# Kernel optimization log

Measured on AMD Instinct MI355X. Metric: run time of the kernel, lower is better.

Reference implementation:

```python
import jax, jax.numpy as jnp
import numpy as np
import math

B, L, D, H = 2, 2048, 1024, 16
DK = D // H

def setup_inputs() -> dict:
    key = jax.random.key(0)
    ks = jax.random.split(key, 12)
    s = 1.0 / math.sqrt(D)
    inp = {
        "Q": jax.random.normal(ks[0], (B, L, D), jnp.float32),
        "K": jax.random.normal(ks[1], (B, L, D), jnp.float32),
        "V": jax.random.normal(ks[2], (B, L, D), jnp.float32),
        "mask": jnp.tril(jnp.ones((L, L), jnp.bool_))[None, None],  # [1,1,L,L] causal
        "Wq_w": jax.random.normal(ks[3], (D, D), jnp.float32) * s,
        "Wq_b": jnp.zeros((D,), jnp.float32),
        "Wk_w": jax.random.normal(ks[4], (D, D), jnp.float32) * s,
        "Wk_b": jnp.zeros((D,), jnp.float32),
        "Wv_w": jax.random.normal(ks[5], (D, D), jnp.float32) * s,
        "Wv_b": jnp.zeros((D,), jnp.float32),
        "fc_w": jax.random.normal(ks[6], (D, D), jnp.float32) * s,
        "fc_b": jnp.zeros((D,), jnp.float32),
    }
    return inp

def reference(Q, K, V, mask, Wq_w, Wq_b, Wk_w, Wk_b, Wv_w, Wv_b, fc_w, fc_b):
    # torch Linear: y = x @ W.T + b
    def split_heads(x):
        return x.reshape(B, L, H, DK).transpose(0, 2, 1, 3)  # [B,H,L,DK]
    q = split_heads(Q @ Wq_w.T + Wq_b)
    k = split_heads(K @ Wk_w.T + Wk_b)
    v = split_heads(V @ Wv_w.T + Wv_b)
    scores = jnp.einsum("bhqd,bhkd->bhqk", q, k) / math.sqrt(DK)
    scores = jnp.where(mask, scores, jnp.float32(-1e9))
    attn = jax.nn.softmax(scores, axis=-1)
    out = jnp.einsum("bhqk,bhkd->bhqd", attn, v)
    out = out.transpose(0, 2, 1, 3).reshape(B, L, D)
    return out @ fc_w.T + fc_b
```

## Files before the change

### kernel.cpp

```cpp
#include <hip/hip_runtime.h>
#include <hip/hip_bf16.h>
#include <math.h>

typedef __attribute__((ext_vector_type(8))) short short8;
typedef __attribute__((ext_vector_type(4))) short short4v;
typedef __attribute__((ext_vector_type(4))) float float4v;
typedef __attribute__((ext_vector_type(2))) unsigned int uint2v;

static constexpr int Bc = 2, Lc = 2048, Dc = 1024, Hc = 16;
static constexpr float C1 = 0.125f * 1.44269504088896f;
static constexpr float C2 = -8.0f * 1.44269504088896f;

__device__ __forceinline__ short f2bf(float x) {
    unsigned int b = __float_as_uint(x);
    return (short)((b + 0x7FFFu + ((b >> 16) & 1u)) >> 16);
}

__device__ __forceinline__ void gld16(const void* g, void* l) {
    __builtin_amdgcn_global_load_lds(
        (const __attribute__((address_space(1))) unsigned int*)g,
        (__attribute__((address_space(3))) unsigned int*)l, 16, 0, 0);
}

__global__ __launch_bounds__(256) void cvt_all(
    const float* q, const float* k, const float* v,
    const float* wq, const float* wk, const float* wv, const float* fw,
    short* qo, short* ko, short* vo,
    short* wqo, short* wko, short* wvo, short* fwo)
{
    const int z = blockIdx.y;
    const float* s; short* d; int n;
    switch (z) {
        case 0: s = q;  d = qo;  n = Bc*Lc*Dc; break;
        case 1: s = k;  d = ko;  n = Bc*Lc*Dc; break;
        case 2: s = v;  d = vo;  n = Bc*Lc*Dc; break;
        case 3: s = wq; d = wqo; n = Dc*Dc; break;
        case 4: s = wk; d = wko; n = Dc*Dc; break;
        case 5: s = wv; d = wvo; n = Dc*Dc; break;
        default: s = fw; d = fwo; n = Dc*Dc; break;
    }
    const int idx = (blockIdx.x * 256 + threadIdx.x) * 8;
    if (idx >= n) return;
    float4 lo = *reinterpret_cast<const float4*>(s + idx);
    float4 hi = *reinterpret_cast<const float4*>(s + idx + 4);
    short8 o = short8{f2bf(lo.x), f2bf(lo.y), f2bf(lo.z), f2bf(lo.w),
                      f2bf(hi.x), f2bf(hi.y), f2bf(hi.z), f2bf(hi.w)};
    *reinterpret_cast<short8*>(d + idx) = o;
}

struct GemmCtx {
    int lane, w, wm, wn, quad, l16, bm0, bn0, lrow, loct;
};
__device__ __forceinline__ void gemm_core(
    const short* __restrict__ A, const short* __restrict__ Bt,
    short* As, short* Bs, const GemmCtx& c, float4v acc[4][4])
{
    const int K = Dc;
    for (int k0 = 0; k0 < K; k0 += 32) {
#pragma unroll
        for (int rep = 0; rep < 2; ++rep) {
            const int rb = (c.w + 4 * rep) * 16;
            gld16(A  + (size_t)(c.bm0 + rb + c.lrow) * K + k0 + c.loct * 8, &As[rb * 32]);
            gld16(Bt + (size_t)(c.bn0 + rb + c.lrow) * K + k0 + c.loct * 8, &Bs[rb * 32]);
        }
        __syncthreads();
        short8 af[4], bf[4];
#pragma unroll
        for (int i = 0; i < 4; ++i)
            af[i] = *reinterpret_cast<const short8*>(&As[(c.wm * 64 + i * 16 + c.l16) * 32 + c.quad * 8]);
#pragma unroll
        for (int j = 0; j < 4; ++j)
            bf[j] = *reinterpret_cast<const short8*>(&Bs[(c.wn * 64 + j * 16 + c.l16) * 32 + c.quad * 8]);
#pragma unroll
        for (int i = 0; i < 4; ++i)
#pragma unroll
            for (int j = 0; j < 4; ++j)
                acc[i][j] = __builtin_amdgcn_mfma_f32_16x16x32_bf16(af[i], bf[j], acc[i][j], 0, 0, 0);
        __syncthreads();
    }
}
__device__ __forceinline__ GemmCtx make_ctx() {
    GemmCtx c;
    const int tid = threadIdx.x;
    c.lane = tid & 63; c.w = tid >> 6;
    c.wm = c.w >> 1;   c.wn = c.w & 1;
    c.quad = c.lane >> 4; c.l16 = c.lane & 15;
    c.bm0 = blockIdx.y * 128; c.bn0 = blockIdx.x * 128;
    c.lrow = c.lane >> 2; c.loct = c.lane & 3;
    return c;
}

__global__ __launch_bounds__(256, 2) void qkv_gemm(
    const short* __restrict__ Qb, const short* __restrict__ Kb, const short* __restrict__ Vb,
    const short* __restrict__ Wq, const short* __restrict__ Wk, const short* __restrict__ Wv,
    const float* __restrict__ bq, const float* __restrict__ bk, const float* __restrict__ bv,
    short* __restrict__ q_ws, short* __restrict__ k_ws, short* __restrict__ vT_ws)
{
    __shared__ short As[128 * 32];
    __shared__ short Bs[128 * 32];
    const int z = blockIdx.z;
    const short* A    = (z == 0) ? Qb : (z == 1) ? Kb : Vb;
    const short* Bt   = (z == 0) ? Wq : (z == 1) ? Wk : Wv;
    const float* bias = (z == 0) ? bq : (z == 1) ? bk : bv;

    GemmCtx c = make_ctx();
    float4v acc[4][4] = {};
    gemm_core(A, Bt, As, Bs, c, acc);

    if (z < 2) {
        short* C = (z == 0) ? q_ws : k_ws;
#pragma unroll
        for (int j = 0; j < 4; ++j) {
            const int col = c.bn0 + c.wn * 64 + j * 16 + c.l16;
            const float bv2 = bias[col];
#pragma unroll
            for (int i = 0; i < 4; ++i)
#pragma unroll
                for (int r = 0; r < 4; ++r) {
                    const int row = c.bm0 + c.wm * 64 + i * 16 + c.quad * 4 + r;
                    C[(size_t)row * Dc + col] = f2bf(acc[i][j][r] + bv2);
                }
        }
    } else {
#pragma unroll
        for (int j = 0; j < 4; ++j) {
            const int col = c.bn0 + c.wn * 64 + j * 16 + c.l16;
            const float bv2 = bias[col];
            const int hh = col >> 6, d = col & 63;
#pragma unroll
            for (int i = 0; i < 4; ++i) {
                const int row0 = c.bm0 + c.wm * 64 + i * 16 + c.quad * 4;
                const int bb = row0 >> 11, l = row0 & 2047;
                short4v o4;
#pragma unroll
                for (int r = 0; r < 4; ++r) o4[r] = f2bf(acc[i][j][r] + bv2);
                *reinterpret_cast<short4v*>(
                    &vT_ws[((size_t)((bb * 16 + hh) * 64 + d)) * Lc + l]) = o4;
            }
        }
    }
}

__global__ __launch_bounds__(256, 2) void out_gemm(
    const short* __restrict__ A, const short* __restrict__ Bt,
    const float* __restrict__ bias, float* __restrict__ C)
{
    __shared__ short As[128 * 32];
    __shared__ short Bs[128 * 32];
    GemmCtx c = make_ctx();
    float4v acc[4][4] = {};
    gemm_core(A, Bt, As, Bs, c, acc);
#pragma unroll
    for (int j = 0; j < 4; ++j) {
        const int col = c.bn0 + c.wn * 64 + j * 16 + c.l16;
        const float bv2 = bias[col];
#pragma unroll
        for (int i = 0; i < 4; ++i)
#pragma unroll
            for (int r = 0; r < 4; ++r) {
                const int row = c.bm0 + c.wm * 64 + i * 16 + c.quad * 4 + r;
                C[(size_t)row * Dc + col] = acc[i][j][r] + bv2;
            }
    }
}

__global__ __launch_bounds__(256, 4) void attn_flash5(
    const short* __restrict__ q_ws,
    const short* __restrict__ k_ws,
    const short* __restrict__ vT_ws,
    short* __restrict__ o_ws)
{
    __shared__ short Ks[2][64 * 64];
    __shared__ short Vs[2][64 * 64];

    const int tid  = threadIdx.x;
    const int lane = tid & 63;
    const int w    = tid >> 6;
    const int quad = lane >> 4;
    const int l16  = lane & 15;
    const int l7   = l16 & 7;

    const int id = blockIdx.x;
    const int g  = id >> 8;
    const int s  = (id >> 5) & 7;
    const int bh = id & 31;
    const int qi = (g == 0) ? (31 - s) : (g == 1) ? (23 - s)
                 : (g == 2) ? s        : (8 + s);
    const int b  = bh >> 4, h = bh & 15;

    const int srow = lane >> 3;
    const int soct = lane & 7;
    const size_t khead  = (size_t)(b * Lc) * Dc + h * 64;
    const size_t vthead = (size_t)(bh * 64) * Lc;
    const int xoct0 = quad ^ l7;
    const int xoct1 = (4 + quad) ^ l7;

    const short onev = (l16 == 0) ? (short)0x3F80 : (short)0;
    const short4v vb4 = short4v{onev, onev, onev, onev};

    auto stage = [&](int tile, int buf) {
#pragma unroll
        for (int rep = 0; rep < 2; ++rep) {
            const int issue = w * 2 + rep;
            const int grow = issue * 8 + srow;
            const int goct = soct ^ (grow & 7);
            gld16(k_ws + khead + (size_t)(tile * 64 + grow) * Dc + goct * 8,
                  &Ks[buf][issue * 512]);
            gld16(vT_ws + vthead + (size_t)grow * Lc + tile * 64 + goct * 8,
                  &Vs[buf][issue * 512]);
        }
    };

    const int q0   = qi * 64;
    const int qw0  = q0 + w * 16;
    const int qrow = qw0 + l16;

    short8 qf[2];
    {
        const size_t base = ((size_t)(b * Lc + qw0 + l16)) * Dc + h * 64;
        qf[0] = *reinterpret_cast<const short8*>(&q_ws[base + quad * 8]);
        qf[1] = *reinterpret_cast<const short8*>(&q_ws[base + 32 + quad * 8]);
    }

    float4v o_acc[5] = {};

    stage(0, 0);

#pragma unroll 1
    for (int kb = 0; kb <= qi; ++kb) {
        const int cur = kb & 1;
        if (kb < qi) {
            stage(kb + 1, cur ^ 1);
            asm volatile("s_waitcnt vmcnt(4)" ::: "memory");
        } else {
            asm volatile("s_waitcnt vmcnt(0)" ::: "memory");
        }
        __builtin_amdgcn_s_barrier();
        asm volatile("" ::: "memory");

        const short* Kc = &Ks[cur][0];
        const short* Vc = &Vs[cur][0];

#pragma unroll
        for (int t = 0; t < 4; ++t) {
            if (kb * 64 + t * 16 <= qw0 + 15) {
                short8 kf0 = *reinterpret_cast<const short8*>(&Kc[(t * 16 + l16) * 64 + xoct0 * 8]);
                short8 kf1 = *reinterpret_cast<const short8*>(&Kc[(t * 16 + l16) * 64 + xoct1 * 8]);
                float4v sv = {};
                sv = __builtin_amdgcn_mfma_f32_16x16x32_bf16(kf0, qf[0], sv, 0, 0, 0);
                sv = __builtin_amdgcn_mfma_f32_16x16x32_bf16(kf1, qf[1], sv, 0, 0, 0);

                short4v vb[4];
#pragma unroll
                for (int dt = 0; dt < 4; ++dt)
                    vb[dt] = *reinterpret_cast<const short4v*>(
                        &Vc[(dt * 16 + l16) * 64 + ((2 * t + (quad >> 1)) ^ l7) * 8 + (quad & 1) * 4]);

                const int kbase = kb * 64 + t * 16 + quad * 4;
                unsigned u[4];
                if (kb * 64 + t * 16 + 15 <= qw0) {
#pragma unroll
                    for (int r = 0; r < 4; ++r)
                        u[r] = __float_as_uint(exp2f(fmaf(sv[r], C1, C2)));
                } else {
#pragma unroll
                    for (int r = 0; r < 4; ++r) {
                        const float pv = (kbase + r <= qrow)
                                       ? exp2f(fmaf(sv[r], C1, C2)) : 0.f;
                        u[r] = __float_as_uint(pv);
                    }
                }
                const uint2v pu = {(u[1] & 0xFFFF0000u) | (u[0] >> 16),
                                   (u[3] & 0xFFFF0000u) | (u[2] >> 16)};
                const short4v pa = __builtin_bit_cast(short4v, pu);

#pragma unroll
                for (int dt = 0; dt < 4; ++dt)
                    o_acc[dt] = __builtin_amdgcn_mfma_f32_16x16x16bf16_1k(pa, vb[dt], o_acc[dt], 0, 0, 0);
                o_acc[4] = __builtin_amdgcn_mfma_f32_16x16x16bf16_1k(pa, vb4, o_acc[4], 0, 0, 0);
            }
        }
        asm volatile("" ::: "memory");
        __builtin_amdgcn_s_barrier();
    }

#pragma unroll
    for (int r = 0; r < 4; ++r) {
        const float lsum = __shfl(o_acc[4][r], quad << 4, 64);
        const float inv = 1.f / lsum;
        const int qr = qw0 + quad * 4 + r;
#pragma unroll
        for (int dt = 0; dt < 4; ++dt)
            o_ws[((size_t)(b * Lc + qr)) * Dc + h * 64 + dt * 16 + l16] =
                f2bf(o_acc[dt][r] * inv);
    }
}

extern "C" void kernel_launch(void* const* d_in, const int* in_sizes, int n_in,
                              void* d_out, int out_size, void* d_ws, size_t ws_size,
                              hipStream_t stream)
{
    const float* Q = (const float*)d_in[0];
    const float* K = (const float*)d_in[1];
    const float* V = (const float*)d_in[2];

    int w0 = -1;
    for (int i = 3; i + 8 <= n_in; ++i) {
        bool ok = true;
        for (int j = 0; j < 4 && ok; ++j)
            ok = (in_sizes[i + 2 * j] == Dc * Dc) && (in_sizes[i + 2 * j + 1] == Dc);
        if (ok) { w0 = i; break; }
    }
    if (w0 < 0) w0 = (n_in >= 12) ? 4 : 3;

    const float* Wq_w = (const float*)d_in[w0 + 0];
    const float* Wq_b = (const float*)d_in[w0 + 1];
    const float* Wk_w = (const float*)d_in[w0 + 2];
    const float* Wk_b = (const float*)d_in[w0 + 3];
    const float* Wv_w = (const float*)d_in[w0 + 4];
    const float* Wv_b = (const float*)d_in[w0 + 5];
    const float* fc_w = (const float*)d_in[w0 + 6];
    const float* fc_b = (const float*)d_in[w0 + 7];
    float* out = (float*)d_out;

    const size_t nel = (size_t)Bc * Lc * Dc;
    const size_t nw  = (size_t)Dc * Dc;
    short* p = (short*)d_ws;
    short* xq   = p;  p += nel;
    short* xk   = p;  p += nel;
    short* xv   = p;  p += nel;
    short* wqb  = p;  p += nw;
    short* wkb  = p;  p += nw;
    short* wvb  = p;  p += nw;
    short* fwb  = p;  p += nw;
    short* q_ws = p;  p += nel;
    short* k_ws = p;  p += nel;
    short* vT_ws= p;  p += nel;
    short* a_ws = xq;

    cvt_all<<<dim3(2048, 7), 256, 0, stream>>>(
        Q, K, V, Wq_w, Wk_w, Wv_w, fc_w, xq, xk, xv, wqb, wkb, wvb, fwb);

    qkv_gemm<<<dim3(8, 32, 3), 256, 0, stream>>>(
        xq, xk, xv, wqb, wkb, wvb, Wq_b, Wk_b, Wv_b, q_ws, k_ws, vT_ws);

    attn_flash5<<<dim3(1024), 256, 0, stream>>>(q_ws, k_ws, vT_ws, a_ws);

    out_gemm<<<dim3(8, 32), 256, 0, stream>>>(a_ws, fwb, fc_b, out);
}
```

Measured before the change: 234.7 us.

## Split attention key tiles across two wave groups and shrink GEMM N-tile

The attention kernel now runs 512 threads in two 4-wave groups. Each group processes alternating 64-key tiles into its own LDS buffer, and the partial outputs and row sums are combined through LDS at the end. This replaces the single-group double-buffered prefetch loop, adding parallelism per query tile but dropping the load/compute overlap. Separately, the QKV and output GEMMs move from 128x128 to 128x64 tiles with a higher occupancy hint, doubling the block count to fill the GPU better at the cost of more A-tile reloads. The tighter launch bounds (512 threads, 8 blocks) may squeeze registers.

```diff
diff --git a/kernel.cpp b/kernel.cpp
--- a/kernel.cpp
+++ b/kernel.cpp
@@ -51,30 +51,31 @@
 struct GemmCtx {
     int lane, w, wm, wn, quad, l16, bm0, bn0, lrow, loct;
 };
-__device__ __forceinline__ void gemm_core(
+__device__ __forceinline__ void gemm_core64(
     const short* __restrict__ A, const short* __restrict__ Bt,
-    short* As, short* Bs, const GemmCtx& c, float4v acc[4][4])
+    short* As, short* Bs, const GemmCtx& c, float4v acc[4][2])
 {
     const int K = Dc;
     for (int k0 = 0; k0 < K; k0 += 32) {
 #pragma unroll
         for (int rep = 0; rep < 2; ++rep) {
             const int rb = (c.w + 4 * rep) * 16;
-            gld16(A  + (size_t)(c.bm0 + rb + c.lrow) * K + k0 + c.loct * 8, &As[rb * 32]);
-            gld16(Bt + (size_t)(c.bn0 + rb + c.lrow) * K + k0 + c.loct * 8, &Bs[rb * 32]);
-        }
+            gld16(A + (size_t)(c.bm0 + rb + c.lrow) * K + k0 + c.loct * 8, &As[rb * 32]);
+        }
+        gld16(Bt + (size_t)(c.bn0 + c.w * 16 + c.lrow) * K + k0 + c.loct * 8,
+              &Bs[c.w * 16 * 32]);
         __syncthreads();
-        short8 af[4], bf[4];
+        short8 af[4], bf[2];
 #pragma unroll
         for (int i = 0; i < 4; ++i)
             af[i] = *reinterpret_cast<const short8*>(&As[(c.wm * 64 + i * 16 + c.l16) * 32 + c.quad * 8]);
 #pragma unroll
-        for (int j = 0; j < 4; ++j)
-            bf[j] = *reinterpret_cast<const short8*>(&Bs[(c.wn * 64 + j * 16 + c.l16) * 32 + c.quad * 8]);
+        for (int j = 0; j < 2; ++j)
+            bf[j] = *reinterpret_cast<const short8*>(&Bs[(c.wn * 32 + j * 16 + c.l16) * 32 + c.quad * 8]);
 #pragma unroll
         for (int i = 0; i < 4; ++i)
 #pragma unroll
-            for (int j = 0; j < 4; ++j)
+            for (int j = 0; j < 2; ++j)
                 acc[i][j] = __builtin_amdgcn_mfma_f32_16x16x32_bf16(af[i], bf[j], acc[i][j], 0, 0, 0);
         __syncthreads();
     }
@@ -85,33 +86,33 @@
     c.lane = tid & 63; c.w = tid >> 6;
     c.wm = c.w >> 1;   c.wn = c.w & 1;
     c.quad = c.lane >> 4; c.l16 = c.lane & 15;
-    c.bm0 = blockIdx.y * 128; c.bn0 = blockIdx.x * 128;
+    c.bm0 = blockIdx.y * 128; c.bn0 = blockIdx.x * 64;
     c.lrow = c.lane >> 2; c.loct = c.lane & 3;
     return c;
 }
 
-__global__ __launch_bounds__(256, 2) void qkv_gemm(
+__global__ __launch_bounds__(256, 4) void qkv_gemm(
     const short* __restrict__ Qb, const short* __restrict__ Kb, const short* __restrict__ Vb,
     const short* __restrict__ Wq, const short* __restrict__ Wk, const short* __restrict__ Wv,
     const float* __restrict__ bq, const float* __restrict__ bk, const float* __restrict__ bv,
     short* __restrict__ q_ws, short* __restrict__ k_ws, short* __restrict__ vT_ws)
 {
     __shared__ short As[128 * 32];
-    __shared__ short Bs[128 * 32];
+    __shared__ short Bs[64 * 32];
     const int z = blockIdx.z;
     const short* A    = (z == 0) ? Qb : (z == 1) ? Kb : Vb;
     const short* Bt   = (z == 0) ? Wq : (z == 1) ? Wk : Wv;
     const float* bias = (z == 0) ? bq : (z == 1) ? bk : bv;
 
     GemmCtx c = make_ctx();
-    float4v acc[4][4] = {};
-    gemm_core(A, Bt, As, Bs, c, acc);
+    float4v acc[4][2] = {};
+    gemm_core64(A, Bt, As, Bs, c, acc);
 
     if (z < 2) {
         short* C = (z == 0) ? q_ws : k_ws;
 #pragma unroll
-        for (int j = 0; j < 4; ++j) {
-            const int col = c.bn0 + c.wn * 64 + j * 16 + c.l16;
+        for (int j = 0; j < 2; ++j) {
+            const int col = c.bn0 + c.wn * 32 + j * 16 + c.l16;
             const float bv2 = bias[col];
 #pragma unroll
             for (int i = 0; i < 4; ++i)
@@ -123,8 +124,8 @@
         }
     } else {
 #pragma unroll
-        for (int j = 0; j < 4; ++j) {
-            const int col = c.bn0 + c.wn * 64 + j * 16 + c.l16;
+        for (int j = 0; j < 2; ++j) {
+            const int col = c.bn0 + c.wn * 32 + j * 16 + c.l16;
             const float bv2 = bias[col];
             const int hh = col >> 6, d = col & 63;
 #pragma unroll
@@ -141,18 +142,18 @@
     }
 }
 
-__global__ __launch_bounds__(256, 2) void out_gemm(
+__global__ __launch_bounds__(256, 4) void out_gemm(
     const short* __restrict__ A, const short* __restrict__ Bt,
     const float* __restrict__ bias, float* __restrict__ C)
 {
     __shared__ short As[128 * 32];
-    __shared__ short Bs[128 * 32];
+    __shared__ short Bs[64 * 32];
     GemmCtx c = make_ctx();
-    float4v acc[4][4] = {};
-    gemm_core(A, Bt, As, Bs, c, acc);
-#pragma unroll
-    for (int j = 0; j < 4; ++j) {
-        const int col = c.bn0 + c.wn * 64 + j * 16 + c.l16;
+    float4v acc[4][2] = {};
+    gemm_core64(A, Bt, As, Bs, c, acc);
+#pragma unroll
+    for (int j = 0; j < 2; ++j) {
+        const int col = c.bn0 + c.wn * 32 + j * 16 + c.l16;
         const float bv2 = bias[col];
 #pragma unroll
         for (int i = 0; i < 4; ++i)
@@ -164,18 +165,19 @@
     }
 }
 
-__global__ __launch_bounds__(256, 4) void attn_flash5(
+__global__ __launch_bounds__(512, 8) void attn_flash6(
     const short* __restrict__ q_ws,
     const short* __restrict__ k_ws,
     const short* __restrict__ vT_ws,
     short* __restrict__ o_ws)
 {
-    __shared__ short Ks[2][64 * 64];
-    __shared__ short Vs[2][64 * 64];
+    __shared__ __align__(16) short KVs[2][2][64 * 64];
 
     const int tid  = threadIdx.x;
     const int lane = tid & 63;
     const int w    = tid >> 6;
+    const int grp  = w >> 2;
+    const int wq   = w & 3;
     const int quad = lane >> 4;
     const int l16  = lane & 15;
     const int l7   = l16 & 7;
@@ -198,21 +200,21 @@
     const short onev = (l16 == 0) ? (short)0x3F80 : (short)0;
     const short4v vb4 = short4v{onev, onev, onev, onev};
 
-    auto stage = [&](int tile, int buf) {
+    auto stage = [&](int tile) {
 #pragma unroll
         for (int rep = 0; rep < 2; ++rep) {
-            const int issue = w * 2 + rep;
+            const int issue = wq * 2 + rep;
             const int grow = issue * 8 + srow;
             const int goct = soct ^ (grow & 7);
             gld16(k_ws + khead + (size_t)(tile * 64 + grow) * Dc + goct * 8,
-                  &Ks[buf][issue * 512]);
+                  &KVs[grp][0][issue * 512]);
             gld16(vT_ws + vthead + (size_t)grow * Lc + tile * 64 + goct * 8,
-                  &Vs[buf][issue * 512]);
+                  &KVs[grp][1][issue * 512]);
         }
     };
 
     const int q0   = qi * 64;
-    const int qw0  = q0 + w * 16;
+    const int qw0  = q0 + wq * 16;
     const int qrow = qw0 + l16;
 
     short8 qf[2];
@@ -224,22 +226,18 @@
 
     float4v o_acc[5] = {};
 
-    stage(0, 0);
+    const int nsi = (qi >> 1) + 1;
 
 #pragma unroll 1
-    for (int kb = 0; kb <= qi; ++kb) {
-        const int cur = kb & 1;
-        if (kb < qi) {
-            stage(kb + 1, cur ^ 1);
-            asm volatile("s_waitcnt vmcnt(4)" ::: "memory");
-        } else {
-            asm volatile("s_waitcnt vmcnt(0)" ::: "memory");
-        }
+    for (int si = 0; si < nsi; ++si) {
+        const int kb = 2 * si + grp;
+        stage(kb);
+        asm volatile("s_waitcnt vmcnt(0)" ::: "memory");
         __builtin_amdgcn_s_barrier();
         asm volatile("" ::: "memory");
 
-        const short* Kc = &Ks[cur][0];
-        const short* Vc = &Vs[cur][0];
+        const short* Kc = &KVs[grp][0][0];
+        const short* Vc = &KVs[grp][1][0];
 
 #pragma unroll
         for (int t = 0; t < 4; ++t) {
@@ -284,15 +282,27 @@
         __builtin_amdgcn_s_barrier();
     }
 
-#pragma unroll
-    for (int r = 0; r < 4; ++r) {
-        const float lsum = __shfl(o_acc[4][r], quad << 4, 64);
-        const float inv = 1.f / lsum;
-        const int qr = qw0 + quad * 4 + r;
-#pragma unroll
-        for (int dt = 0; dt < 4; ++dt)
-            o_ws[((size_t)(b * Lc + qr)) * Dc + h * 64 + dt * 16 + l16] =
-                f2bf(o_acc[dt][r] * inv);
+    float4v* cmbv = reinterpret_cast<float4v*>(&KVs[0][0][0]);
+    if (grp == 1) {
+#pragma unroll
+        for (int dt = 0; dt < 5; ++dt)
+            cmbv[dt * 256 + wq * 64 + lane] = o_acc[dt];
+    }
+    __syncthreads();
+    if (grp == 0) {
+#pragma unroll
+        for (int dt = 0; dt < 5; ++dt)
+            o_acc[dt] += cmbv[dt * 256 + wq * 64 + lane];
+#pragma unroll
+        for (int r = 0; r < 4; ++r) {
+            const float lsum = __shfl(o_acc[4][r], quad << 4, 64);
+            const float inv = 1.f / lsum;
+            const int qr = qw0 + quad * 4 + r;
+#pragma unroll
+            for (int dt = 0; dt < 4; ++dt)
+                o_ws[((size_t)(b * Lc + qr)) * Dc + h * 64 + dt * 16 + l16] =
+                    f2bf(o_acc[dt][r] * inv);
+        }
     }
 }
 
@@ -341,10 +351,10 @@
     cvt_all<<<dim3(2048, 7), 256, 0, stream>>>(
         Q, K, V, Wq_w, Wk_w, Wv_w, fc_w, xq, xk, xv, wqb, wkb, wvb, fwb);
 
-    qkv_gemm<<<dim3(8, 32, 3), 256, 0, stream>>>(
+    qkv_gemm<<<dim3(16, 32, 3), 256, 0, stream>>>(
         xq, xk, xv, wqb, wkb, wvb, Wq_b, Wk_b, Wv_b, q_ws, k_ws, vT_ws);
 
-    attn_flash5<<<dim3(1024), 256, 0, stream>>>(q_ws, k_ws, vT_ws, a_ws);
-
-    out_gemm<<<dim3(8, 32), 256, 0, stream>>>(a_ws, fwb, fc_b, out);
-}
+    attn_flash6<<<dim3(1024), 512, 0, stream>>>(q_ws, k_ws, vT_ws, a_ws);
+
+    out_gemm<<<dim3(16, 32), 256, 0, stream>>>(a_ws, fwb, fc_b, out);
+}
```

After: 255.0 us. +8.6%, slower.

## Split long causal attention rows across two blocks and combine partial sums

Applied to the files above, without the earlier changes.

Query tiles in the upper half (qi>=16) now have their key range split between two blocks. Each block writes unnormalized partial accumulators and row sums to a float workspace, and a new combine kernel adds the two halves and normalizes. This works because the softmax uses a fixed max offset, so partials add directly. The change also separates full off-diagonal tiles from the diagonal tile so the mask check only runs on the diagonal, raises launch bounds to 5 blocks, and adds s_setprio around MFMA groups. The cost is an extra kernel launch plus the global round-trip for the partials, in exchange for less tail imbalance across the grid.

```diff
diff --git a/kernel.cpp b/kernel.cpp
--- a/kernel.cpp
+++ b/kernel.cpp
@@ -164,11 +164,12 @@
     }
 }
 
-__global__ __launch_bounds__(256, 4) void attn_flash5(
+__global__ __launch_bounds__(256, 5) void attn_flash8(
     const short* __restrict__ q_ws,
     const short* __restrict__ k_ws,
     const short* __restrict__ vT_ws,
-    short* __restrict__ o_ws)
+    short* __restrict__ o_ws,
+    float4v* __restrict__ pbuf)
 {
     __shared__ short Ks[2][64 * 64];
     __shared__ short Vs[2][64 * 64];
@@ -181,12 +182,18 @@
     const int l7   = l16 & 7;
 
     const int id = blockIdx.x;
-    const int g  = id >> 8;
-    const int s  = (id >> 5) & 7;
     const int bh = id & 31;
-    const int qi = (g == 0) ? (31 - s) : (g == 1) ? (23 - s)
-                 : (g == 2) ? s        : (8 + s);
-    const int b  = bh >> 4, h = bh & 15;
+    const int c  = id >> 5;
+    int qi, start, cnt, half, two;
+    if (c % 3 == 2) {
+        qi = 15 - c / 3; start = 0; cnt = qi + 1; half = 0; two = 0;
+    } else {
+        const int di = (c / 3) * 2 + (c % 3);
+        qi = 31 - (di >> 1); half = di & 1;
+        const int n = qi + 1, c0 = (n + 1) >> 1;
+        start = half ? c0 : 0; cnt = half ? (n - c0) : c0; two = 1;
+    }
+    const int b = bh >> 4, h = bh & 15;
 
     const int srow = lane >> 3;
     const int soct = lane & 7;
@@ -224,12 +231,13 @@
 
     float4v o_acc[5] = {};
 
-    stage(0, 0);
+    stage(start, 0);
+    const int end = start + cnt;
 
 #pragma unroll 1
-    for (int kb = 0; kb <= qi; ++kb) {
-        const int cur = kb & 1;
-        if (kb < qi) {
+    for (int kb = start; kb < end; ++kb) {
+        const int cur = (kb - start) & 1;
+        if (kb + 1 < end) {
             stage(kb + 1, cur ^ 1);
             asm volatile("s_waitcnt vmcnt(4)" ::: "memory");
         } else {
@@ -241,14 +249,16 @@
         const short* Kc = &Ks[cur][0];
         const short* Vc = &Vs[cur][0];
 
-#pragma unroll
-        for (int t = 0; t < 4; ++t) {
-            if (kb * 64 + t * 16 <= qw0 + 15) {
+        if (kb < qi) {
+#pragma unroll
+            for (int t = 0; t < 4; ++t) {
                 short8 kf0 = *reinterpret_cast<const short8*>(&Kc[(t * 16 + l16) * 64 + xoct0 * 8]);
                 short8 kf1 = *reinterpret_cast<const short8*>(&Kc[(t * 16 + l16) * 64 + xoct1 * 8]);
+                __builtin_amdgcn_s_setprio(1);
                 float4v sv = {};
                 sv = __builtin_amdgcn_mfma_f32_16x16x32_bf16(kf0, qf[0], sv, 0, 0, 0);
                 sv = __builtin_amdgcn_mfma_f32_16x16x32_bf16(kf1, qf[1], sv, 0, 0, 0);
+                __builtin_amdgcn_s_setprio(0);
 
                 short4v vb[4];
 #pragma unroll
@@ -256,43 +266,111 @@
                     vb[dt] = *reinterpret_cast<const short4v*>(
                         &Vc[(dt * 16 + l16) * 64 + ((2 * t + (quad >> 1)) ^ l7) * 8 + (quad & 1) * 4]);
 
-                const int kbase = kb * 64 + t * 16 + quad * 4;
                 unsigned u[4];
-                if (kb * 64 + t * 16 + 15 <= qw0) {
-#pragma unroll
-                    for (int r = 0; r < 4; ++r)
-                        u[r] = __float_as_uint(exp2f(fmaf(sv[r], C1, C2)));
-                } else {
-#pragma unroll
-                    for (int r = 0; r < 4; ++r) {
-                        const float pv = (kbase + r <= qrow)
-                                       ? exp2f(fmaf(sv[r], C1, C2)) : 0.f;
-                        u[r] = __float_as_uint(pv);
-                    }
-                }
+#pragma unroll
+                for (int r = 0; r < 4; ++r)
+                    u[r] = __float_as_uint(exp2f(fmaf(sv[r], C1, C2)));
                 const uint2v pu = {(u[1] & 0xFFFF0000u) | (u[0] >> 16),
                                    (u[3] & 0xFFFF0000u) | (u[2] >> 16)};
                 const short4v pa = __builtin_bit_cast(short4v, pu);
 
+                __builtin_amdgcn_s_setprio(1);
 #pragma unroll
                 for (int dt = 0; dt < 4; ++dt)
                     o_acc[dt] = __builtin_amdgcn_mfma_f32_16x16x16bf16_1k(pa, vb[dt], o_acc[dt], 0, 0, 0);
                 o_acc[4] = __builtin_amdgcn_mfma_f32_16x16x16bf16_1k(pa, vb4, o_acc[4], 0, 0, 0);
+                __builtin_amdgcn_s_setprio(0);
+            }
+        } else {
+#pragma unroll
+            for (int t = 0; t < 4; ++t) {
+                if (t <= w) {
+                    short8 kf0 = *reinterpret_cast<const short8*>(&Kc[(t * 16 + l16) * 64 + xoct0 * 8]);
+                    short8 kf1 = *reinterpret_cast<const short8*>(&Kc[(t * 16 + l16) * 64 + xoct1 * 8]);
+                    float4v sv = {};
+                    sv = __builtin_amdgcn_mfma_f32_16x16x32_bf16(kf0, qf[0], sv, 0, 0, 0);
+                    sv = __builtin_amdgcn_mfma_f32_16x16x32_bf16(kf1, qf[1], sv, 0, 0, 0);
+
+                    short4v vb[4];
+#pragma unroll
+                    for (int dt = 0; dt < 4; ++dt)
+                        vb[dt] = *reinterpret_cast<const short4v*>(
+                            &Vc[(dt * 16 + l16) * 64 + ((2 * t + (quad >> 1)) ^ l7) * 8 + (quad & 1) * 4]);
+
+                    const int kbase = kb * 64 + t * 16 + quad * 4;
+                    unsigned u[4];
+                    if (t < w) {
+#pragma unroll
+                        for (int r = 0; r < 4; ++r)
+                            u[r] = __float_as_uint(exp2f(fmaf(sv[r], C1, C2)));
+                    } else {
+#pragma unroll
+                        for (int r = 0; r < 4; ++r) {
+                            const float pv = (kbase + r <= qrow)
+                                           ? exp2f(fmaf(sv[r], C1, C2)) : 0.f;
+                            u[r] = __float_as_uint(pv);
+                        }
+                    }
+                    const uint2v pu = {(u[1] & 0xFFFF0000u) | (u[0] >> 16),
+                                       (u[3] & 0xFFFF0000u) | (u[2] >> 16)};
+                    const short4v pa = __builtin_bit_cast(short4v, pu);
+
+#pragma unroll
+                    for (int dt = 0; dt < 4; ++dt)
+                        o_acc[dt] = __builtin_amdgcn_mfma_f32_16x16x16bf16_1k(pa, vb[dt], o_acc[dt], 0, 0, 0);
+                    o_acc[4] = __builtin_amdgcn_mfma_f32_16x16x16bf16_1k(pa, vb4, o_acc[4], 0, 0, 0);
+                }
             }
         }
         asm volatile("" ::: "memory");
         __builtin_amdgcn_s_barrier();
     }
 
+    if (!two) {
+#pragma unroll
+        for (int r = 0; r < 4; ++r) {
+            const float lsum = __shfl(o_acc[4][r], quad << 4, 64);
+            const float inv = 1.f / lsum;
+            const int qr = qw0 + quad * 4 + r;
+#pragma unroll
+            for (int dt = 0; dt < 4; ++dt)
+                o_ws[((size_t)(b * Lc + qr)) * Dc + h * 64 + dt * 16 + l16] =
+                    f2bf(o_acc[dt][r] * inv);
+        }
+    } else {
+        const size_t sb = ((size_t)((bh * 16 + (qi - 16)) * 2 + half)) * 1280 + tid;
+#pragma unroll
+        for (int dt = 0; dt < 5; ++dt)
+            pbuf[sb + dt * 256] = o_acc[dt];
+    }
+}
+
+__global__ __launch_bounds__(256) void attn_combine(
+    const float4v* __restrict__ pbuf, short* __restrict__ o_ws)
+{
+    const int id  = blockIdx.x;
+    const int tid = threadIdx.x;
+    const int lane = tid & 63, w = tid >> 6;
+    const int quad = lane >> 4, l16 = lane & 15;
+    const int bh = id >> 4, t2 = id & 15, qi = 16 + t2;
+    const int b = bh >> 4, h = bh & 15;
+
+    const size_t s0 = (size_t)id * 2560 + tid;
+    float4v o[5];
+#pragma unroll
+    for (int dt = 0; dt < 5; ++dt)
+        o[dt] = pbuf[s0 + dt * 256] + pbuf[s0 + 1280 + dt * 256];
+
+    const int qw0 = qi * 64 + w * 16;
 #pragma unroll
     for (int r = 0; r < 4; ++r) {
-        const float lsum = __shfl(o_acc[4][r], quad << 4, 64);
+        const float lsum = __shfl(o[4][r], quad << 4, 64);
         const float inv = 1.f / lsum;
         const int qr = qw0 + quad * 4 + r;
 #pragma unroll
         for (int dt = 0; dt < 4; ++dt)
             o_ws[((size_t)(b * Lc + qr)) * Dc + h * 64 + dt * 16 + l16] =
-                f2bf(o_acc[dt][r] * inv);
+                f2bf(o[dt][r] * inv);
     }
 }
 
@@ -337,6 +415,7 @@
     short* k_ws = p;  p += nel;
     short* vT_ws= p;  p += nel;
     short* a_ws = xq;
+    float4v* pbuf = (float4v*)xk;
 
     cvt_all<<<dim3(2048, 7), 256, 0, stream>>>(
         Q, K, V, Wq_w, Wk_w, Wv_w, fc_w, xq, xk, xv, wqb, wkb, wvb, fwb);
@@ -344,7 +423,9 @@
     qkv_gemm<<<dim3(8, 32, 3), 256, 0, stream>>>(
         xq, xk, xv, wqb, wkb, wvb, Wq_b, Wk_b, Wv_b, q_ws, k_ws, vT_ws);
 
-    attn_flash5<<<dim3(1024), 256, 0, stream>>>(q_ws, k_ws, vT_ws, a_ws);
+    attn_flash8<<<dim3(1536), 256, 0, stream>>>(q_ws, k_ws, vT_ws, a_ws, pbuf);
+
+    attn_combine<<<dim3(512), 256, 0, stream>>>(pbuf, a_ws);
 
     out_gemm<<<dim3(8, 32), 256, 0, stream>>>(a_ws, fwb, fc_b, out);
 }
```

Result: slower. 246.4 us (+5.0%).

## Double GEMM K-tile to 64 with XOR-swizzled LDS and split attention diagonal path

Applied to the files above, without the earlier changes.

The GEMM core now stages 64-wide K slices per iteration with an XOR swizzle on the LDS octet index, halving the number of barrier pairs and aiming to avoid bank conflicts on the fragment reads. LDS use per GEMM block doubles, which may affect occupancy. The attention kernel splits off-diagonal key blocks into a branch-free path and handles the diagonal block separately, using the wave index to decide which subtiles are full, partial or skipped. This removes per-subtile causal checks from the common loop at the cost of a larger, duplicated code body.

```diff
diff --git a/kernel.cpp b/kernel.cpp
--- a/kernel.cpp
+++ b/kernel.cpp
@@ -49,33 +49,43 @@
 }
 
 struct GemmCtx {
-    int lane, w, wm, wn, quad, l16, bm0, bn0, lrow, loct;
+    int lane, w, wm, wn, quad, l16, bm0, bn0, srow, soct;
 };
 __device__ __forceinline__ void gemm_core(
     const short* __restrict__ A, const short* __restrict__ Bt,
     short* As, short* Bs, const GemmCtx& c, float4v acc[4][4])
 {
     const int K = Dc;
-    for (int k0 = 0; k0 < K; k0 += 32) {
-#pragma unroll
-        for (int rep = 0; rep < 2; ++rep) {
-            const int rb = (c.w + 4 * rep) * 16;
-            gld16(A  + (size_t)(c.bm0 + rb + c.lrow) * K + k0 + c.loct * 8, &As[rb * 32]);
-            gld16(Bt + (size_t)(c.bn0 + rb + c.lrow) * K + k0 + c.loct * 8, &Bs[rb * 32]);
+    const int l7 = c.l16 & 7;
+    for (int k0 = 0; k0 < K; k0 += 64) {
+#pragma unroll
+        for (int rep = 0; rep < 4; ++rep) {
+            const int rb = (c.w * 4 + rep) * 8;
+            const int goct = c.soct ^ c.srow;
+            gld16(A  + (size_t)(c.bm0 + rb + c.srow) * K + k0 + goct * 8,
+                  &As[rb * 64]);
+            gld16(Bt + (size_t)(c.bn0 + rb + c.srow) * K + k0 + goct * 8,
+                  &Bs[rb * 64]);
         }
         __syncthreads();
-        short8 af[4], bf[4];
-#pragma unroll
-        for (int i = 0; i < 4; ++i)
-            af[i] = *reinterpret_cast<const short8*>(&As[(c.wm * 64 + i * 16 + c.l16) * 32 + c.quad * 8]);
-#pragma unroll
-        for (int j = 0; j < 4; ++j)
-            bf[j] = *reinterpret_cast<const short8*>(&Bs[(c.wn * 64 + j * 16 + c.l16) * 32 + c.quad * 8]);
-#pragma unroll
-        for (int i = 0; i < 4; ++i)
+#pragma unroll
+        for (int s = 0; s < 2; ++s) {
+            const int roct = (s * 4 + c.quad) ^ l7;
+            short8 af[4], bf[4];
+#pragma unroll
+            for (int i = 0; i < 4; ++i)
+                af[i] = *reinterpret_cast<const short8*>(
+                    &As[(c.wm * 64 + i * 16 + c.l16) * 64 + roct * 8]);
 #pragma unroll
             for (int j = 0; j < 4; ++j)
-                acc[i][j] = __builtin_amdgcn_mfma_f32_16x16x32_bf16(af[i], bf[j], acc[i][j], 0, 0, 0);
+                bf[j] = *reinterpret_cast<const short8*>(
+                    &Bs[(c.wn * 64 + j * 16 + c.l16) * 64 + roct * 8]);
+#pragma unroll
+            for (int i = 0; i < 4; ++i)
+#pragma unroll
+                for (int j = 0; j < 4; ++j)
+                    acc[i][j] = __builtin_amdgcn_mfma_f32_16x16x32_bf16(af[i], bf[j], acc[i][j], 0, 0, 0);
+        }
         __syncthreads();
     }
 }
@@ -86,7 +96,7 @@
     c.wm = c.w >> 1;   c.wn = c.w & 1;
     c.quad = c.lane >> 4; c.l16 = c.lane & 15;
     c.bm0 = blockIdx.y * 128; c.bn0 = blockIdx.x * 128;
-    c.lrow = c.lane >> 2; c.loct = c.lane & 3;
+    c.srow = c.lane >> 3; c.soct = c.lane & 7;
     return c;
 }
 
@@ -96,8 +106,8 @@
     const float* __restrict__ bq, const float* __restrict__ bk, const float* __restrict__ bv,
     short* __restrict__ q_ws, short* __restrict__ k_ws, short* __restrict__ vT_ws)
 {
-    __shared__ short As[128 * 32];
-    __shared__ short Bs[128 * 32];
+    __shared__ short As[128 * 64];
+    __shared__ short Bs[128 * 64];
     const int z = blockIdx.z;
     const short* A    = (z == 0) ? Qb : (z == 1) ? Kb : Vb;
     const short* Bt   = (z == 0) ? Wq : (z == 1) ? Wk : Wv;
@@ -145,8 +155,8 @@
     const short* __restrict__ A, const short* __restrict__ Bt,
     const float* __restrict__ bias, float* __restrict__ C)
 {
-    __shared__ short As[128 * 32];
-    __shared__ short Bs[128 * 32];
+    __shared__ short As[128 * 64];
+    __shared__ short Bs[128 * 64];
     GemmCtx c = make_ctx();
     float4v acc[4][4] = {};
     gemm_core(A, Bt, As, Bs, c, acc);
@@ -164,7 +174,7 @@
     }
 }
 
-__global__ __launch_bounds__(256, 4) void attn_flash5(
+__global__ __launch_bounds__(256, 4) void attn_flash7(
     const short* __restrict__ q_ws,
     const short* __restrict__ k_ws,
     const short* __restrict__ vT_ws,
@@ -241,9 +251,9 @@
         const short* Kc = &Ks[cur][0];
         const short* Vc = &Vs[cur][0];
 
-#pragma unroll
-        for (int t = 0; t < 4; ++t) {
-            if (kb * 64 + t * 16 <= qw0 + 15) {
+        if (kb < qi) {
+#pragma unroll
+            for (int t = 0; t < 4; ++t) {
                 short8 kf0 = *reinterpret_cast<const short8*>(&Kc[(t * 16 + l16) * 64 + xoct0 * 8]);
                 short8 kf1 = *reinterpret_cast<const short8*>(&Kc[(t * 16 + l16) * 64 + xoct1 * 8]);
                 float4v sv = {};
@@ -256,20 +266,10 @@
                     vb[dt] = *reinterpret_cast<const short4v*>(
                         &Vc[(dt * 16 + l16) * 64 + ((2 * t + (quad >> 1)) ^ l7) * 8 + (quad & 1) * 4]);
 
-                const int kbase = kb * 64 + t * 16 + quad * 4;
                 unsigned u[4];
-                if (kb * 64 + t * 16 + 15 <= qw0) {
-#pragma unroll
-                    for (int r = 0; r < 4; ++r)
-                        u[r] = __float_as_uint(exp2f(fmaf(sv[r], C1, C2)));
-                } else {
-#pragma unroll
-                    for (int r = 0; r < 4; ++r) {
-                        const float pv = (kbase + r <= qrow)
-                                       ? exp2f(fmaf(sv[r], C1, C2)) : 0.f;
-                        u[r] = __float_as_uint(pv);
-                    }
-                }
+#pragma unroll
+                for (int r = 0; r < 4; ++r)
+                    u[r] = __float_as_uint(exp2f(fmaf(sv[r], C1, C2)));
                 const uint2v pu = {(u[1] & 0xFFFF0000u) | (u[0] >> 16),
                                    (u[3] & 0xFFFF0000u) | (u[2] >> 16)};
                 const short4v pa = __builtin_bit_cast(short4v, pu);
@@ -278,6 +278,46 @@
                 for (int dt = 0; dt < 4; ++dt)
                     o_acc[dt] = __builtin_amdgcn_mfma_f32_16x16x16bf16_1k(pa, vb[dt], o_acc[dt], 0, 0, 0);
                 o_acc[4] = __builtin_amdgcn_mfma_f32_16x16x16bf16_1k(pa, vb4, o_acc[4], 0, 0, 0);
+            }
+        } else {
+#pragma unroll
+            for (int t = 0; t < 4; ++t) {
+                if (t <= w) {
+                    short8 kf0 = *reinterpret_cast<const short8*>(&Kc[(t * 16 + l16) * 64 + xoct0 * 8]);
+                    short8 kf1 = *reinterpret_cast<const short8*>(&Kc[(t * 16 + l16) * 64 + xoct1 * 8]);
+                    float4v sv = {};
+                    sv = __builtin_amdgcn_mfma_f32_16x16x32_bf16(kf0, qf[0], sv, 0, 0, 0);
+                    sv = __builtin_amdgcn_mfma_f32_16x16x32_bf16(kf1, qf[1], sv, 0, 0, 0);
+
+                    short4v vb[4];
+#pragma unroll
+                    for (int dt = 0; dt < 4; ++dt)
+                        vb[dt] = *reinterpret_cast<const short4v*>(
+                            &Vc[(dt * 16 + l16) * 64 + ((2 * t + (quad >> 1)) ^ l7) * 8 + (quad & 1) * 4]);
+
+                    const int kbase = kb * 64 + t * 16 + quad * 4;
+                    unsigned u[4];
+                    if (t < w) {
+#pragma unroll
+                        for (int r = 0; r < 4; ++r)
+                            u[r] = __float_as_uint(exp2f(fmaf(sv[r], C1, C2)));
+                    } else {
+#pragma unroll
+                        for (int r = 0; r < 4; ++r) {
+                            const float pv = (kbase + r <= qrow)
+                                           ? exp2f(fmaf(sv[r], C1, C2)) : 0.f;
+                            u[r] = __float_as_uint(pv);
+                        }
+                    }
+                    const uint2v pu = {(u[1] & 0xFFFF0000u) | (u[0] >> 16),
+                                       (u[3] & 0xFFFF0000u) | (u[2] >> 16)};
+                    const short4v pa = __builtin_bit_cast(short4v, pu);
+
+#pragma unroll
+                    for (int dt = 0; dt < 4; ++dt)
+                        o_acc[dt] = __builtin_amdgcn_mfma_f32_16x16x16bf16_1k(pa, vb[dt], o_acc[dt], 0, 0, 0);
+                    o_acc[4] = __builtin_amdgcn_mfma_f32_16x16x16bf16_1k(pa, vb4, o_acc[4], 0, 0, 0);
+                }
             }
         }
         asm volatile("" ::: "memory");
@@ -344,7 +384,7 @@
     qkv_gemm<<<dim3(8, 32, 3), 256, 0, stream>>>(
         xq, xk, xv, wqb, wkb, wvb, Wq_b, Wk_b, Wv_b, q_ws, k_ws, vT_ws);
 
-    attn_flash5<<<dim3(1024), 256, 0, stream>>>(q_ws, k_ws, vT_ws, a_ws);
+    attn_flash7<<<dim3(1024), 256, 0, stream>>>(q_ws, k_ws, vT_ws, a_ws);
 
     out_gemm<<<dim3(8, 32), 256, 0, stream>>>(a_ws, fwb, fc_b, out);
 }
```

After: 226.4 us. 1.04x faster.
